# Performance work log

Hardware: AMD Instinct MI355X
Metric: run time of the kernel (lower is better)

## Reference

```python
import jax, jax.numpy as jnp
import numpy as np

NEG_SLOPE = 0.2

def _leaky_relu(x):
    return jnp.where(x >= 0, x, NEG_SLOPE * x)

def setup_inputs() -> dict:
    key = jax.random.key(0)
    ks = jax.random.split(key, 12)
    B, N, M = 64, 4096, 128
    d_ope, d_ma, d_out = 6, 3, 8
    return {
        "ope_ma_adj": jax.random.randint(ks[0], (B, N, M), 0, 2, dtype=jnp.int32),
        "batch_idxes": jnp.arange(B, dtype=jnp.int32),
        "ope_feat": jax.random.normal(ks[1], (B, N, d_ope), dtype=jnp.float32),
        "ma_feat": jax.random.normal(ks[2], (B, M, d_ma), dtype=jnp.float32),
        "proc_time": jax.random.uniform(ks[3], (B, N, M), dtype=jnp.float32),
        "W_src": jax.random.normal(ks[4], (d_ope, d_out), dtype=jnp.float32),
        "W_dst": jax.random.normal(ks[5], (d_ma, d_out), dtype=jnp.float32),
        "w_edge": jax.random.normal(ks[6], (d_out,), dtype=jnp.float32),
        "attn_l": jax.random.normal(ks[7], (d_out,), dtype=jnp.float32),
        "attn_r": jax.random.normal(ks[8], (d_out,), dtype=jnp.float32),
        "attn_e": jax.random.normal(ks[9], (d_out,), dtype=jnp.float32),
    }

def reference(ope_ma_adj, batch_idxes, ope_feat, ma_feat, proc_time,
              W_src, W_dst, w_edge, attn_l, attn_r, attn_e):
    # GATedge.forward with num_head=1 (head dim folded away).
    adj_i = ope_ma_adj[batch_idxes]            # [B,N,M] int (0/1)
    adj = adj_i.astype(jnp.float32)
    feat_src = ope_feat @ W_src                # [B,N,d]
    feat_dst = ma_feat @ W_dst                 # [B,M,d]
    el = feat_src @ attn_l                     # [B,N]
    er = feat_dst @ attn_r                     # [B,M]
    # fc_edge is Linear(1,d): feat_edge = proc[...,None]*w_edge, so
    # ee = (feat_edge*attn_e).sum(-1) = proc * dot(w_edge, attn_e)
    ee = proc_time * jnp.dot(w_edge, attn_e)   # [B,N,M]
    a = adj * el[:, :, None] + ee + adj * er[:, None, :]
    eijk = _leaky_relu(a)                      # [B,N,M]
    ekk = _leaky_relu(2.0 * er)                # [B,M]
    neg_inf = jnp.asarray(-jnp.inf, dtype=eijk.dtype)
    eijk_m = jnp.where(adj_i == 1, eijk, neg_inf)
    e = jnp.concatenate([eijk_m, ekk[:, None, :]], axis=1)   # [B,N+1,M]
    alpha = jax.nn.softmax(e, axis=1)          # softmax over ops (+self)
    alpha_ijk = alpha[:, :-1, :]               # [B,N,M]
    alpha_kk = alpha[:, -1, :]                 # [B,M]
    # b = sum_j alpha_ijk * (feat_edge + feat_src), split to avoid [B,N,M,d]
    b_edge = jnp.einsum('bnm,bnm->bm', alpha_ijk, proc_time)[..., None] * w_edge  # [B,M,d]
    b_src = jnp.einsum('bnm,bnd->bmd', alpha_ijk, feat_src)                       # [B,M,d]
    c = feat_dst * alpha_kk[..., None]         # [B,M,d]
    return jax.nn.sigmoid(b_edge + b_src + c)  # nu_k_prime [B,M,d]
```

## Files before the change

kernel.cpp:

```cpp
#include <hip/hip_runtime.h>
#include <hip/hip_bf16.h>

constexpr int B  = 64;
constexpr int N  = 4096;
constexpr int M  = 128;
constexpr int DO = 8;
constexpr int NC = 32;
constexpr int CH = N / NC;
constexpr int TR = 8;
constexpr int NT = CH / TR;
constexpr float CEXP = 20.0f;

typedef __attribute__((address_space(3))) void       lds_void;
typedef const __attribute__((address_space(1))) void gbl_void;

__global__ __launch_bounds__(256) void hgnn_k1(
    const int*   __restrict__ adj,
    const int*   __restrict__ bidx,
    const float* __restrict__ ope_feat,
    const float* __restrict__ ma_feat,
    const float* __restrict__ proc,
    const float* __restrict__ W_src,
    const float* __restrict__ W_dst,
    const float* __restrict__ w_edge,
    const float* __restrict__ attn_l,
    const float* __restrict__ attn_r,
    const float* __restrict__ attn_e,
    float*       __restrict__ part)
{
    const int chunk = blockIdx.x;
    const int b     = blockIdx.y;
    const int t     = threadIdx.x;
    const int m     = t & 127;
    const int sub   = t >> 7;
    const int w     = t >> 6;
    const int n0    = chunk * CH;

    __shared__ __align__(16) int   bufA[2][TR * M];
    __shared__ __align__(16) float bufP[2][TR * M];
    __shared__ __align__(16) float fs[CH][DO];
    __shared__ float el_s[CH];
    __shared__ float red[M][12];

    const int ab = bidx[b];

    const int elemoff = w * 256 + (t & 63) * 4;
    auto issue_tile = [&](int j, int pq) {
        const int* gA = adj  + ((size_t)ab * N + n0 + (size_t)j * TR) * M + elemoff;
        const float* gP = proc + ((size_t)b * N + n0 + (size_t)j * TR) * M + elemoff;
        __builtin_amdgcn_global_load_lds((gbl_void*)gA,
                                         (lds_void*)&bufA[pq][w * 256], 16, 0, 0);
        __builtin_amdgcn_global_load_lds((gbl_void*)gP,
                                         (lds_void*)&bufP[pq][w * 256], 16, 0, 0);
    };

    issue_tile(0, 0);

    float er = 0.f;
    {
        const float* mf = ma_feat + ((size_t)b * M + m) * 3;
        const float f0 = mf[0], f1 = mf[1], f2 = mf[2];
#pragma unroll
        for (int d = 0; d < DO; ++d) {
            const float fd = f0 * W_dst[d] + f1 * W_dst[DO + d] + f2 * W_dst[2 * DO + d];
            er += fd * attn_r[d];
        }
    }
    float cee = 0.f;
#pragma unroll
    for (int d = 0; d < DO; ++d) cee += w_edge[d] * attn_e[d];

    if (t < CH) {
        const float* of = ope_feat + ((size_t)b * N + (n0 + t)) * 6;
        const float o0 = of[0], o1 = of[1], o2 = of[2], o3 = of[3], o4 = of[4], o5 = of[5];
        float el = 0.f;
#pragma unroll
        for (int d = 0; d < DO; ++d) {
            const float f = o0 * W_src[d] + o1 * W_src[DO + d] + o2 * W_src[2 * DO + d] +
                            o3 * W_src[3 * DO + d] + o4 * W_src[4 * DO + d] + o5 * W_src[5 * DO + d];
            fs[t][d] = f;
            el += f * attn_l[d];
        }
        el_s[t] = el;
    }

    float l = 0.f, sp = 0.f;
    float sf[DO];
#pragma unroll
    for (int d = 0; d < DO; ++d) sf[d] = 0.f;

    for (int j = 0; j < NT; ++j) {
        __syncthreads();
        if (j + 1 < NT) issue_tile(j + 1, (j + 1) & 1);
        __syncthreads();

        const int pq = j & 1;
#pragma unroll
        for (int k = 0; k < 4; ++k) {
            const int lr = sub * 4 + k;
            const int r  = j * TR + lr;
            const int   a = bufA[pq][lr * M + m];
            const float p = bufP[pq][lr * M + m];
            const float el = el_s[r];
            const float4 f0 = *reinterpret_cast<const float4*>(&fs[r][0]);
            const float4 f1 = *reinterpret_cast<const float4*>(&fs[r][4]);

            float v = el + er + cee * p;
            v = (v >= 0.f) ? v : 0.2f * v;
            const float vm = (a != 0) ? v : -1e30f;
            const float wt = __expf(vm - CEXP);
            l += wt;
            sp = fmaf(wt, p, sp);
            sf[0] = fmaf(wt, f0.x, sf[0]);
            sf[1] = fmaf(wt, f0.y, sf[1]);
            sf[2] = fmaf(wt, f0.z, sf[2]);
            sf[3] = fmaf(wt, f0.w, sf[3]);
            sf[4] = fmaf(wt, f1.x, sf[4]);
            sf[5] = fmaf(wt, f1.y, sf[5]);
            sf[6] = fmaf(wt, f1.z, sf[6]);
            sf[7] = fmaf(wt, f1.w, sf[7]);
        }
    }

    if (sub == 1) {
        red[m][0] = l;
        red[m][1] = sp;
#pragma unroll
        for (int d = 0; d < DO; ++d) red[m][2 + d] = sf[d];
    }
    __syncthreads();
    if (sub == 0) {
        l  += red[m][0];
        sp += red[m][1];
#pragma unroll
        for (int d = 0; d < DO; ++d) sf[d] += red[m][2 + d];

        const size_t stride = (size_t)B * NC * M;
        const size_t base   = ((size_t)b * NC + chunk) * M + m;
        part[base]          = l;
        part[stride + base] = sp;
#pragma unroll
        for (int d = 0; d < DO; ++d) part[(size_t)(2 + d) * stride + base] = sf[d];
    }
}

__global__ __launch_bounds__(256) void hgnn_k2(
    const float* __restrict__ ma_feat,
    const float* __restrict__ W_dst,
    const float* __restrict__ w_edge,
    const float* __restrict__ attn_r,
    const float* __restrict__ part,
    float*       __restrict__ out)
{
    const int t = blockIdx.x * 256 + threadIdx.x;
    if (t >= B * M) return;
    const int m = t & (M - 1);
    const int b = t >> 7;

    const size_t stride = (size_t)B * NC * M;

    float acc[10];
#pragma unroll
    for (int f = 0; f < 10; ++f) acc[f] = 0.f;

    for (int c = 0; c < NC; c += 4) {
        float tmp[4][10];
#pragma unroll
        for (int j = 0; j < 4; ++j) {
            const size_t base = ((size_t)b * NC + (c + j)) * M + m;
#pragma unroll
            for (int f = 0; f < 10; ++f) tmp[j][f] = part[(size_t)f * stride + base];
        }
#pragma unroll
        for (int j = 0; j < 4; ++j)
#pragma unroll
            for (int f = 0; f < 10; ++f) acc[f] += tmp[j][f];
    }

    const float* mf = ma_feat + ((size_t)b * M + m) * 3;
    const float f0 = mf[0], f1 = mf[1], f2 = mf[2];
    float fd[DO];
    float er = 0.f;
#pragma unroll
    for (int d = 0; d < DO; ++d) {
        fd[d] = f0 * W_dst[d] + f1 * W_dst[DO + d] + f2 * W_dst[2 * DO + d];
        er += fd[d] * attn_r[d];
    }
    float ekk = 2.f * er;
    ekk = (ekk >= 0.f) ? ekk : 0.2f * ekk;
    const float wkk = __expf(ekk - CEXP);

    const float L    = acc[0] + wkk;
    const float invL = 1.f / L;
    const float akk  = wkk * invL;
    const float spf  = acc[1] * invL;

#pragma unroll
    for (int d = 0; d < DO; ++d) {
        const float x = spf * w_edge[d] + acc[2 + d] * invL + fd[d] * akk;
        out[(size_t)t * DO + d] = 1.f / (1.f + __expf(-x));
    }
}

extern "C" void kernel_launch(void* const* d_in, const int* in_sizes, int n_in,
                              void* d_out, int out_size, void* d_ws, size_t ws_size,
                              hipStream_t stream) {
    const int*   adj      = (const int*)  d_in[0];
    const int*   bidx     = (const int*)  d_in[1];
    const float* ope_feat = (const float*)d_in[2];
    const float* ma_feat  = (const float*)d_in[3];
    const float* proc     = (const float*)d_in[4];
    const float* W_src    = (const float*)d_in[5];
    const float* W_dst    = (const float*)d_in[6];
    const float* w_edge   = (const float*)d_in[7];
    const float* attn_l   = (const float*)d_in[8];
    const float* attn_r   = (const float*)d_in[9];
    const float* attn_e   = (const float*)d_in[10];
    float* out  = (float*)d_out;
    float* part = (float*)d_ws;

    hgnn_k1<<<dim3(NC, B), 256, 0, stream>>>(adj, bidx, ope_feat, ma_feat, proc,
                                             W_src, W_dst, w_edge, attn_l, attn_r,
                                             attn_e, part);
    hgnn_k2<<<dim3((B * M + 255) / 256), 256, 0, stream>>>(ma_feat, W_dst, w_edge,
                                                           attn_r, part, out);
}
```

Baseline: 309.4 us.

## Per-wave 4-deep async load pipeline with waitcnt and atomic cross-chunk reduction

Each wave now owns a contiguous quarter of the row chunk and streams its own 2-row tiles through a 4-stage ring of LDS buffers. It uses explicit vmcnt waits instead of two block-wide barriers per tile, and each thread handles two columns. The cross-chunk partial sums are reduced inside the block and combined with global atomicAdd into a zeroed accumulator, which removes the large partial buffer and the loop in the second kernel. This adds a memset launch and atomic contention, and makes float summation order nondeterministic.

```diff
diff --git a/kernel.cpp b/kernel.cpp
--- a/kernel.cpp
+++ b/kernel.cpp
@@ -7,9 +7,11 @@
 constexpr int DO = 8;
 constexpr int NC = 32;
 constexpr int CH = N / NC;
-constexpr int TR = 8;
-constexpr int NT = CH / TR;
+constexpr int RW = CH / 4;
+constexpr int NS = RW / 2;
 constexpr float CEXP = 20.0f;
+
+constexpr int waitimm(int n) { return (n & 15) | ((n >> 4) << 14) | (7 << 4) | (15 << 8); }
 
 typedef __attribute__((address_space(3))) void       lds_void;
 typedef const __attribute__((address_space(1))) void gbl_void;
@@ -26,49 +28,36 @@
     const float* __restrict__ attn_l,
     const float* __restrict__ attn_r,
     const float* __restrict__ attn_e,
-    float*       __restrict__ part)
+    float*       __restrict__ acc)
 {
     const int chunk = blockIdx.x;
     const int b     = blockIdx.y;
     const int t     = threadIdx.x;
-    const int m     = t & 127;
-    const int sub   = t >> 7;
     const int w     = t >> 6;
+    const int lane  = t & 63;
     const int n0    = chunk * CH;
 
-    __shared__ __align__(16) int   bufA[2][TR * M];
-    __shared__ __align__(16) float bufP[2][TR * M];
+    __shared__ __align__(16) int   bufA[4][4][256];
+    __shared__ __align__(16) float bufP[4][4][256];
     __shared__ __align__(16) float fs[CH][DO];
     __shared__ float el_s[CH];
-    __shared__ float red[M][12];
-
-    const int ab = bidx[b];
-
-    const int elemoff = w * 256 + (t & 63) * 4;
-    auto issue_tile = [&](int j, int pq) {
-        const int* gA = adj  + ((size_t)ab * N + n0 + (size_t)j * TR) * M + elemoff;
-        const float* gP = proc + ((size_t)b * N + n0 + (size_t)j * TR) * M + elemoff;
-        __builtin_amdgcn_global_load_lds((gbl_void*)gA,
-                                         (lds_void*)&bufA[pq][w * 256], 16, 0, 0);
-        __builtin_amdgcn_global_load_lds((gbl_void*)gP,
-                                         (lds_void*)&bufP[pq][w * 256], 16, 0, 0);
-    };
-
-    issue_tile(0, 0);
-
-    float er = 0.f;
+
+    const int c0 = lane;
+    const int c1 = lane + 64;
+
+    float er0 = 0.f, er1 = 0.f, cee = 0.f;
     {
-        const float* mf = ma_feat + ((size_t)b * M + m) * 3;
-        const float f0 = mf[0], f1 = mf[1], f2 = mf[2];
+        const float* mf0 = ma_feat + ((size_t)b * M + c0) * 3;
+        const float* mf1 = ma_feat + ((size_t)b * M + c1) * 3;
+        const float a0 = mf0[0], a1 = mf0[1], a2 = mf0[2];
+        const float b0 = mf1[0], b1 = mf1[1], b2 = mf1[2];
 #pragma unroll
         for (int d = 0; d < DO; ++d) {
-            const float fd = f0 * W_dst[d] + f1 * W_dst[DO + d] + f2 * W_dst[2 * DO + d];
-            er += fd * attn_r[d];
-        }
-    }
-    float cee = 0.f;
-#pragma unroll
-    for (int d = 0; d < DO; ++d) cee += w_edge[d] * attn_e[d];
+            er0 += (a0 * W_dst[d] + a1 * W_dst[DO + d] + a2 * W_dst[2 * DO + d]) * attn_r[d];
+            er1 += (b0 * W_dst[d] + b1 * W_dst[DO + d] + b2 * W_dst[2 * DO + d]) * attn_r[d];
+            cee += w_edge[d] * attn_e[d];
+        }
+    }
 
     if (t < CH) {
         const float* of = ope_feat + ((size_t)b * N + (n0 + t)) * 6;
@@ -83,64 +72,113 @@
         }
         el_s[t] = el;
     }
-
-    float l = 0.f, sp = 0.f;
-    float sf[DO];
-#pragma unroll
-    for (int d = 0; d < DO; ++d) sf[d] = 0.f;
-
-    for (int j = 0; j < NT; ++j) {
-        __syncthreads();
-        if (j + 1 < NT) issue_tile(j + 1, (j + 1) & 1);
-        __syncthreads();
-
-        const int pq = j & 1;
-#pragma unroll
-        for (int k = 0; k < 4; ++k) {
-            const int lr = sub * 4 + k;
-            const int r  = j * TR + lr;
-            const int   a = bufA[pq][lr * M + m];
-            const float p = bufP[pq][lr * M + m];
-            const float el = el_s[r];
+    __syncthreads();
+
+    const int ab = bidx[b];
+    const int*   adjw  = adj  + ((size_t)ab * N + n0 + w * RW) * M;
+    const float* procw = proc + ((size_t)b  * N + n0 + w * RW) * M;
+    const int l4 = lane * 4;
+
+    auto issue = [&](int S) {
+        __builtin_amdgcn_global_load_lds((gbl_void*)(adjw + (size_t)S * 256 + l4),
+                                         (lds_void*)&bufA[w][S & 3][0], 16, 0, 0);
+        __builtin_amdgcn_global_load_lds((gbl_void*)(procw + (size_t)S * 256 + l4),
+                                         (lds_void*)&bufP[w][S & 3][0], 16, 0, 0);
+    };
+
+    float l0 = 0.f, sp0 = 0.f, l1 = 0.f, sp1 = 0.f;
+    float sf0[DO], sf1[DO];
+#pragma unroll
+    for (int d = 0; d < DO; ++d) { sf0[d] = 0.f; sf1[d] = 0.f; }
+
+    auto consume = [&](int S) {
+        const int sb = (S & 3) * 256;
+        const int* bA = &bufA[w][0][0];
+        const float* bP = &bufP[w][0][0];
+#pragma unroll
+        for (int rr = 0; rr < 2; ++rr) {
+            const int r = w * RW + S * 2 + rr;
+            const float  el = el_s[r];
             const float4 f0 = *reinterpret_cast<const float4*>(&fs[r][0]);
             const float4 f1 = *reinterpret_cast<const float4*>(&fs[r][4]);
-
-            float v = el + er + cee * p;
-            v = (v >= 0.f) ? v : 0.2f * v;
-            const float vm = (a != 0) ? v : -1e30f;
-            const float wt = __expf(vm - CEXP);
-            l += wt;
-            sp = fmaf(wt, p, sp);
-            sf[0] = fmaf(wt, f0.x, sf[0]);
-            sf[1] = fmaf(wt, f0.y, sf[1]);
-            sf[2] = fmaf(wt, f0.z, sf[2]);
-            sf[3] = fmaf(wt, f0.w, sf[3]);
-            sf[4] = fmaf(wt, f1.x, sf[4]);
-            sf[5] = fmaf(wt, f1.y, sf[5]);
-            sf[6] = fmaf(wt, f1.z, sf[6]);
-            sf[7] = fmaf(wt, f1.w, sf[7]);
-        }
-    }
-
-    if (sub == 1) {
-        red[m][0] = l;
-        red[m][1] = sp;
-#pragma unroll
-        for (int d = 0; d < DO; ++d) red[m][2 + d] = sf[d];
-    }
-    __syncthreads();
-    if (sub == 0) {
-        l  += red[m][0];
-        sp += red[m][1];
-#pragma unroll
-        for (int d = 0; d < DO; ++d) sf[d] += red[m][2 + d];
-
-        const size_t stride = (size_t)B * NC * M;
-        const size_t base   = ((size_t)b * NC + chunk) * M + m;
-        part[base]          = l;
-        part[stride + base] = sp;
-#pragma unroll
-        for (int d = 0; d < DO; ++d) part[(size_t)(2 + d) * stride + base] = sf[d];
+            const int   a0 = bA[sb + rr * 128 + c0];
+            const int   a1 = bA[sb + rr * 128 + c1];
+            const float p0 = bP[sb + rr * 128 + c0];
+            const float p1 = bP[sb + rr * 128 + c1];
+            {
+                float v = el + er0 + cee * p0;
+                v = (v >= 0.f) ? v : 0.2f * v;
+                const float wt = __expf(((a0 != 0) ? v : -1e30f) - CEXP);
+                l0 += wt; sp0 = fmaf(wt, p0, sp0);
+                sf0[0] = fmaf(wt, f0.x, sf0[0]); sf0[1] = fmaf(wt, f0.y, sf0[1]);
+                sf0[2] = fmaf(wt, f0.z, sf0[2]); sf0[3] = fmaf(wt, f0.w, sf0[3]);
+                sf0[4] = fmaf(wt, f1.x, sf0[4]); sf0[5] = fmaf(wt, f1.y, sf0[5]);
+                sf0[6] = fmaf(wt, f1.z, sf0[6]); sf0[7] = fmaf(wt, f1.w, sf0[7]);
+            }
+            {
+                float v = el + er1 + cee * p1;
+                v = (v >= 0.f) ? v : 0.2f * v;
+                const float wt = __expf(((a1 != 0) ? v : -1e30f) - CEXP);
+                l1 += wt; sp1 = fmaf(wt, p1, sp1);
+                sf1[0] = fmaf(wt, f0.x, sf1[0]); sf1[1] = fmaf(wt, f0.y, sf1[1]);
+                sf1[2] = fmaf(wt, f0.z, sf1[2]); sf1[3] = fmaf(wt, f0.w, sf1[3]);
+                sf1[4] = fmaf(wt, f1.x, sf1[4]); sf1[5] = fmaf(wt, f1.y, sf1[5]);
+                sf1[6] = fmaf(wt, f1.z, sf1[6]); sf1[7] = fmaf(wt, f1.w, sf1[7]);
+            }
+        }
+    };
+
+    issue(0); issue(1); issue(2); issue(3);
+
+#define STEP_MI(S) { __builtin_amdgcn_s_waitcnt(waitimm(6)); consume(S); issue((S) + 4); }
+#define STEP_NI(S, WN) { __builtin_amdgcn_s_waitcnt(waitimm(WN)); consume(S); }
+    STEP_MI(0)  STEP_MI(1)  STEP_MI(2)  STEP_MI(3)
+    STEP_MI(4)  STEP_MI(5)  STEP_MI(6)  STEP_MI(7)
+    STEP_MI(8)  STEP_MI(9)  STEP_MI(10) STEP_MI(11)
+    STEP_NI(12, 6) STEP_NI(13, 4) STEP_NI(14, 2) STEP_NI(15, 0)
+#undef STEP_MI
+#undef STEP_NI
+
+    float* R = reinterpret_cast<float*>(&bufA[0][0][0]);
+    const size_t colbase = (size_t)b * M;
+
+    __syncthreads();
+    {
+        float v0[5] = {l0, sp0, sf0[0], sf0[1], sf0[2]};
+        float v1[5] = {l1, sp1, sf1[0], sf1[1], sf1[2]};
+#pragma unroll
+        for (int k = 0; k < 5; ++k) {
+            R[(w * 5 + k) * 128 + c0] = v0[k];
+            R[(w * 5 + k) * 128 + c1] = v1[k];
+        }
+    }
+    __syncthreads();
+    if (t < M) {
+#pragma unroll
+        for (int k = 0; k < 5; ++k) {
+            const float s = R[(0 * 5 + k) * 128 + t] + R[(1 * 5 + k) * 128 + t] +
+                            R[(2 * 5 + k) * 128 + t] + R[(3 * 5 + k) * 128 + t];
+            atomicAdd(&acc[(size_t)k * (B * M) + colbase + t], s);
+        }
+    }
+    __syncthreads();
+    {
+        float v0[5] = {sf0[3], sf0[4], sf0[5], sf0[6], sf0[7]};
+        float v1[5] = {sf1[3], sf1[4], sf1[5], sf1[6], sf1[7]};
+#pragma unroll
+        for (int k = 0; k < 5; ++k) {
+            R[(w * 5 + k) * 128 + c0] = v0[k];
+            R[(w * 5 + k) * 128 + c1] = v1[k];
+        }
+    }
+    __syncthreads();
+    if (t < M) {
+#pragma unroll
+        for (int k = 0; k < 5; ++k) {
+            const float s = R[(0 * 5 + k) * 128 + t] + R[(1 * 5 + k) * 128 + t] +
+                            R[(2 * 5 + k) * 128 + t] + R[(3 * 5 + k) * 128 + t];
+            atomicAdd(&acc[(size_t)(5 + k) * (B * M) + colbase + t], s);
+        }
     }
 }
 
@@ -149,7 +187,7 @@
     const float* __restrict__ W_dst,
     const float* __restrict__ w_edge,
     const float* __restrict__ attn_r,
-    const float* __restrict__ part,
+    const float* __restrict__ acc,
     float*       __restrict__ out)
 {
     const int t = blockIdx.x * 256 + threadIdx.x;
@@ -157,25 +195,9 @@
     const int m = t & (M - 1);
     const int b = t >> 7;
 
-    const size_t stride = (size_t)B * NC * M;
-
-    float acc[10];
-#pragma unroll
-    for (int f = 0; f < 10; ++f) acc[f] = 0.f;
-
-    for (int c = 0; c < NC; c += 4) {
-        float tmp[4][10];
-#pragma unroll
-        for (int j = 0; j < 4; ++j) {
-            const size_t base = ((size_t)b * NC + (c + j)) * M + m;
-#pragma unroll
-            for (int f = 0; f < 10; ++f) tmp[j][f] = part[(size_t)f * stride + base];
-        }
-#pragma unroll
-        for (int j = 0; j < 4; ++j)
-#pragma unroll
-            for (int f = 0; f < 10; ++f) acc[f] += tmp[j][f];
-    }
+    float a[10];
+#pragma unroll
+    for (int f = 0; f < 10; ++f) a[f] = acc[(size_t)f * (B * M) + t];
 
     const float* mf = ma_feat + ((size_t)b * M + m) * 3;
     const float f0 = mf[0], f1 = mf[1], f2 = mf[2];
@@ -190,14 +212,14 @@
     ekk = (ekk >= 0.f) ? ekk : 0.2f * ekk;
     const float wkk = __expf(ekk - CEXP);
 
-    const float L    = acc[0] + wkk;
+    const float L    = a[0] + wkk;
     const float invL = 1.f / L;
     const float akk  = wkk * invL;
-    const float spf  = acc[1] * invL;
+    const float spf  = a[1] * invL;
 
 #pragma unroll
     for (int d = 0; d < DO; ++d) {
-        const float x = spf * w_edge[d] + acc[2 + d] * invL + fd[d] * akk;
+        const float x = spf * w_edge[d] + a[2 + d] * invL + fd[d] * akk;
         out[(size_t)t * DO + d] = 1.f / (1.f + __expf(-x));
     }
 }
@@ -216,12 +238,13 @@
     const float* attn_l   = (const float*)d_in[8];
     const float* attn_r   = (const float*)d_in[9];
     const float* attn_e   = (const float*)d_in[10];
-    float* out  = (float*)d_out;
-    float* part = (float*)d_ws;
-
+    float* out = (float*)d_out;
+    float* acc = (float*)d_ws;
+
+    hipMemsetAsync(acc, 0, (size_t)10 * B * M * sizeof(float), stream);
     hgnn_k1<<<dim3(NC, B), 256, 0, stream>>>(adj, bidx, ope_feat, ma_feat, proc,
                                              W_src, W_dst, w_edge, attn_l, attn_r,
-                                             attn_e, part);
+                                             attn_e, acc);
     hgnn_k2<<<dim3((B * M + 255) / 256), 256, 0, stream>>>(ma_feat, W_dst, w_edge,
-                                                           attn_r, part, out);
+                                                           attn_r, acc, out);
 }
```

Measured after the change: 303.3 us. 2.0% less time.

## Replace LDS double-buffered tiles with register-prefetched dwordx4 loads and shuffle reduction

Applied to the files above, without the earlier changes.

Drops the global_load_lds double buffer and its two __syncthreads per tile. Each thread now handles 4 adjacent machine columns and streams adj/proc rows straight into registers with inline-asm dwordx4 loads, keeping 4 tiles in flight through explicit vmcnt waits. The end-of-block reduction changes to a cross-half-wave shuffle followed by an LDS sum over the 4 waves. This removes barrier stalls and LDS traffic, but raises register pressure (40 accumulators plus 8 vector buffers), and the hand-written waitcnt schedule is fragile.

```diff
diff --git a/kernel.cpp b/kernel.cpp
--- a/kernel.cpp
+++ b/kernel.cpp
@@ -7,12 +7,10 @@
 constexpr int DO = 8;
 constexpr int NC = 32;
 constexpr int CH = N / NC;
-constexpr int TR = 8;
-constexpr int NT = CH / TR;
 constexpr float CEXP = 20.0f;
 
-typedef __attribute__((address_space(3))) void       lds_void;
-typedef const __attribute__((address_space(1))) void gbl_void;
+typedef int   v4i __attribute__((ext_vector_type(4)));
+typedef float v4f __attribute__((ext_vector_type(4)));
 
 __global__ __launch_bounds__(256) void hgnn_k1(
     const int*   __restrict__ adj,
@@ -31,42 +29,28 @@
     const int chunk = blockIdx.x;
     const int b     = blockIdx.y;
     const int t     = threadIdx.x;
-    const int m     = t & 127;
-    const int sub   = t >> 7;
+    const int sub   = t >> 5;
+    const int mq    = t & 31;
+    const int c0    = 4 * mq;
     const int w     = t >> 6;
+    const int lane  = t & 63;
     const int n0    = chunk * CH;
 
-    __shared__ __align__(16) int   bufA[2][TR * M];
-    __shared__ __align__(16) float bufP[2][TR * M];
     __shared__ __align__(16) float fs[CH][DO];
     __shared__ float el_s[CH];
-    __shared__ float red[M][12];
-
-    const int ab = bidx[b];
-
-    const int elemoff = w * 256 + (t & 63) * 4;
-    auto issue_tile = [&](int j, int pq) {
-        const int* gA = adj  + ((size_t)ab * N + n0 + (size_t)j * TR) * M + elemoff;
-        const float* gP = proc + ((size_t)b * N + n0 + (size_t)j * TR) * M + elemoff;
-        __builtin_amdgcn_global_load_lds((gbl_void*)gA,
-                                         (lds_void*)&bufA[pq][w * 256], 16, 0, 0);
-        __builtin_amdgcn_global_load_lds((gbl_void*)gP,
-                                         (lds_void*)&bufP[pq][w * 256], 16, 0, 0);
-    };
-
-    issue_tile(0, 0);
-
-    float er = 0.f;
-    {
-        const float* mf = ma_feat + ((size_t)b * M + m) * 3;
+    __shared__ float red[4][32][42];
+
+    float er4[4], cee = 0.f;
+#pragma unroll
+    for (int ci = 0; ci < 4; ++ci) {
+        const float* mf = ma_feat + ((size_t)b * M + (c0 + ci)) * 3;
         const float f0 = mf[0], f1 = mf[1], f2 = mf[2];
-#pragma unroll
-        for (int d = 0; d < DO; ++d) {
-            const float fd = f0 * W_dst[d] + f1 * W_dst[DO + d] + f2 * W_dst[2 * DO + d];
-            er += fd * attn_r[d];
-        }
-    }
-    float cee = 0.f;
+        float er = 0.f;
+#pragma unroll
+        for (int d = 0; d < DO; ++d)
+            er += (f0 * W_dst[d] + f1 * W_dst[DO + d] + f2 * W_dst[2 * DO + d]) * attn_r[d];
+        er4[ci] = er;
+    }
 #pragma unroll
     for (int d = 0; d < DO; ++d) cee += w_edge[d] * attn_e[d];
 
@@ -83,64 +67,94 @@
         }
         el_s[t] = el;
     }
-
-    float l = 0.f, sp = 0.f;
-    float sf[DO];
-#pragma unroll
-    for (int d = 0; d < DO; ++d) sf[d] = 0.f;
-
-    for (int j = 0; j < NT; ++j) {
-        __syncthreads();
-        if (j + 1 < NT) issue_tile(j + 1, (j + 1) & 1);
-        __syncthreads();
-
-        const int pq = j & 1;
-#pragma unroll
-        for (int k = 0; k < 4; ++k) {
-            const int lr = sub * 4 + k;
-            const int r  = j * TR + lr;
-            const int   a = bufA[pq][lr * M + m];
-            const float p = bufP[pq][lr * M + m];
-            const float el = el_s[r];
-            const float4 f0 = *reinterpret_cast<const float4*>(&fs[r][0]);
-            const float4 f1 = *reinterpret_cast<const float4*>(&fs[r][4]);
-
-            float v = el + er + cee * p;
-            v = (v >= 0.f) ? v : 0.2f * v;
-            const float vm = (a != 0) ? v : -1e30f;
-            const float wt = __expf(vm - CEXP);
-            l += wt;
-            sp = fmaf(wt, p, sp);
-            sf[0] = fmaf(wt, f0.x, sf[0]);
-            sf[1] = fmaf(wt, f0.y, sf[1]);
-            sf[2] = fmaf(wt, f0.z, sf[2]);
-            sf[3] = fmaf(wt, f0.w, sf[3]);
-            sf[4] = fmaf(wt, f1.x, sf[4]);
-            sf[5] = fmaf(wt, f1.y, sf[5]);
-            sf[6] = fmaf(wt, f1.z, sf[6]);
-            sf[7] = fmaf(wt, f1.w, sf[7]);
-        }
-    }
-
-    if (sub == 1) {
-        red[m][0] = l;
-        red[m][1] = sp;
-#pragma unroll
-        for (int d = 0; d < DO; ++d) red[m][2 + d] = sf[d];
-    }
     __syncthreads();
-    if (sub == 0) {
-        l  += red[m][0];
-        sp += red[m][1];
-#pragma unroll
-        for (int d = 0; d < DO; ++d) sf[d] += red[m][2 + d];
-
+
+    const int ab = bidx[b];
+    const int*   gA = adj  + ((size_t)ab * N + n0 + sub) * M + c0;
+    const float* gP = proc + ((size_t)b  * N + n0 + sub) * M + c0;
+
+    float l4[4] = {0.f, 0.f, 0.f, 0.f}, sp4[4] = {0.f, 0.f, 0.f, 0.f};
+    float sf4[4][DO];
+#pragma unroll
+    for (int ci = 0; ci < 4; ++ci)
+#pragma unroll
+        for (int d = 0; d < DO; ++d) sf4[ci][d] = 0.f;
+
+    v4i A[4];
+    v4f P[4];
+
+    auto consume = [&](int j, v4i a, v4f p) {
+        const int r = 8 * j + sub;
+        const float  el = el_s[r];
+        const float4 f0 = *reinterpret_cast<const float4*>(&fs[r][0]);
+        const float4 f1 = *reinterpret_cast<const float4*>(&fs[r][4]);
+#pragma unroll
+        for (int ci = 0; ci < 4; ++ci) {
+            float v = fmaf(cee, p[ci], el + er4[ci]);
+            v = fmaxf(v, 0.2f * v);
+            const float wt = __expf(((a[ci] != 0) ? v : -1e30f) - CEXP);
+            l4[ci] += wt;
+            sp4[ci] = fmaf(wt, p[ci], sp4[ci]);
+            sf4[ci][0] = fmaf(wt, f0.x, sf4[ci][0]);
+            sf4[ci][1] = fmaf(wt, f0.y, sf4[ci][1]);
+            sf4[ci][2] = fmaf(wt, f0.z, sf4[ci][2]);
+            sf4[ci][3] = fmaf(wt, f0.w, sf4[ci][3]);
+            sf4[ci][4] = fmaf(wt, f1.x, sf4[ci][4]);
+            sf4[ci][5] = fmaf(wt, f1.y, sf4[ci][5]);
+            sf4[ci][6] = fmaf(wt, f1.z, sf4[ci][6]);
+            sf4[ci][7] = fmaf(wt, f1.w, sf4[ci][7]);
+        }
+    };
+
+#define ISSUE(J)                                                                   \
+    asm volatile("global_load_dwordx4 %0, %1, off"                                 \
+                 : "=v"(A[(J) & 3]) : "v"(gA + (size_t)(J) * 8 * M));              \
+    asm volatile("global_load_dwordx4 %0, %1, off"                                 \
+                 : "=v"(P[(J) & 3]) : "v"(gP + (size_t)(J) * 8 * M));
+
+#define WAITC(J, NSTR)                                                             \
+    asm volatile("s_waitcnt vmcnt(" NSTR ")" : "+v"(A[(J) & 3]), "+v"(P[(J) & 3]));
+
+#define STEP(J)        { WAITC(J, "6") consume(J, A[(J) & 3], P[(J) & 3]); ISSUE((J) + 4) }
+#define TSTEP(J, NSTR) { WAITC(J, NSTR) consume(J, A[(J) & 3], P[(J) & 3]); }
+
+    ISSUE(0) ISSUE(1) ISSUE(2) ISSUE(3)
+    STEP(0)  STEP(1)  STEP(2)  STEP(3)  STEP(4)  STEP(5)
+    STEP(6)  STEP(7)  STEP(8)  STEP(9)  STEP(10) STEP(11)
+    TSTEP(12, "6") TSTEP(13, "4") TSTEP(14, "2") TSTEP(15, "0")
+
+#undef ISSUE
+#undef WAITC
+#undef STEP
+#undef TSTEP
+
+    float v[40];
+#pragma unroll
+    for (int ci = 0; ci < 4; ++ci) {
+        v[ci * 10 + 0] = l4[ci];
+        v[ci * 10 + 1] = sp4[ci];
+#pragma unroll
+        for (int d = 0; d < DO; ++d) v[ci * 10 + 2 + d] = sf4[ci][d];
+    }
+#pragma unroll
+    for (int f = 0; f < 40; ++f) v[f] += __shfl_down(v[f], 32);
+
+    if (lane < 32) {
+#pragma unroll
+        for (int f = 0; f < 40; ++f) red[w][lane][f] = v[f];
+    }
+    __syncthreads();
+
+    if (t < M) {
+        const int gq = t >> 2, ci = t & 3;
         const size_t stride = (size_t)B * NC * M;
-        const size_t base   = ((size_t)b * NC + chunk) * M + m;
-        part[base]          = l;
-        part[stride + base] = sp;
-#pragma unroll
-        for (int d = 0; d < DO; ++d) part[(size_t)(2 + d) * stride + base] = sf[d];
+        const size_t base   = ((size_t)b * NC + chunk) * M + t;
+#pragma unroll
+        for (int f = 0; f < 10; ++f) {
+            const float s = red[0][gq][ci * 10 + f] + red[1][gq][ci * 10 + f] +
+                            red[2][gq][ci * 10 + f] + red[3][gq][ci * 10 + f];
+            part[(size_t)f * stride + base] = s;
+        }
     }
 }
 
```

Measured after the change: 304.9 us. No clear change (-1.4%).
